# Kernel optimization log

Hardware: AMD Instinct MI355X
Metric: run time of the kernel (lower is better)

The kernel has to match this reference:

```python
import jax, jax.numpy as jnp
import numpy as np

NEG_SLOPE = 0.2
LN_EPS = 1e-5


def _gat(x, src, dst, ea, Wl, Wr, We, att, b, heads, ch, concat):
    # GATv2 conv with edge features (eval mode: dropout = identity).
    N = x.shape[0]
    xl = (x @ Wl).reshape(N, heads, ch)          # source transform (also skip output)
    xr = (x @ Wr).reshape(N, heads, ch)          # target transform
    ee = (ea @ We).reshape(ea.shape[0], heads, ch)
    g = jax.nn.leaky_relu(xl[src] + xr[dst] + ee, NEG_SLOPE)   # [E,H,C]
    score = jnp.einsum('ehc,hc->eh', g, att)                    # [E,H]
    # segment softmax over destination nodes
    smax = jax.ops.segment_max(score, dst, num_segments=N)
    ex = jnp.exp(score - smax[dst])
    den = jax.ops.segment_sum(ex, dst, num_segments=N)
    alpha = ex / (den[dst] + 1e-16)
    out = jax.ops.segment_sum(xl[src] * alpha[..., None], dst, num_segments=N)  # [N,H,C]
    out = out.reshape(N, heads * ch) if concat else out.mean(axis=1)
    return out + b, xl.reshape(N, heads * ch)


def setup_inputs() -> dict:
    B, N, E, F, ED = 4, 20000, 640000, 64, 16
    HID, H1 = 16, 8
    key = jax.random.key(0)
    ks = jax.random.split(key, 32)

    def p(k, shape, fan):
        return (jax.random.normal(k, shape, jnp.float32) / np.float32(np.sqrt(fan)))

    inp = {
        'x': jax.random.normal(ks[0], (B, N, F), jnp.float32),
        'edge_attr': jax.random.normal(ks[1], (B, E, ED), jnp.float32),
        'edge_index': jax.random.randint(ks[2], (B, 2, E), 0, N, jnp.int32),
        # conv1: in=64, heads=8, out=16, concat
        'c1_Wl': p(ks[3], (F, H1 * HID), F),
        'c1_Wr': p(ks[4], (F, H1 * HID), F),
        'c1_We': p(ks[5], (ED, H1 * HID), ED),
        'c1_att': p(ks[6], (H1, HID), HID),
        'c1_b': jnp.zeros((H1 * HID,), jnp.float32),
        # conv2: in=128, heads=1, out=16, mean
        'c2_Wl': p(ks[7], (H1 * HID, HID), H1 * HID),
        'c2_Wr': p(ks[8], (H1 * HID, HID), H1 * HID),
        'c2_We': p(ks[9], (ED, HID), ED),
        'c2_att': p(ks[10], (1, HID), HID),
        'c2_b': jnp.zeros((HID,), jnp.float32),
        # skip_conv: in=128, heads=1, out=16, mean
        's_Wl': p(ks[11], (H1 * HID, HID), H1 * HID),
        's_Wr': p(ks[12], (H1 * HID, HID), H1 * HID),
        's_We': p(ks[13], (ED, HID), ED),
        's_att': p(ks[14], (1, HID), HID),
        's_b': jnp.zeros((HID,), jnp.float32),
        # lin_skip_conv + LayerNorm(16)
        'lin_W': p(ks[15], (HID, HID), HID),
        'lin_b': jnp.zeros((HID,), jnp.float32),
        'ln_g': jnp.ones((HID,), jnp.float32),
        'ln_b': jnp.zeros((HID,), jnp.float32),
    }
    return inp


def reference(x, edge_attr, edge_index,
              c1_Wl, c1_Wr, c1_We, c1_att, c1_b,
              c2_Wl, c2_Wr, c2_We, c2_att, c2_b,
              s_Wl, s_Wr, s_We, s_att, s_b,
              lin_W, lin_b, ln_g, ln_b):
    def single(xg, eig, eag):
        src, dst = eig[0], eig[1]
        h, skip = _gat(xg, src, dst, eag, c1_Wl, c1_Wr, c1_We, c1_att, c1_b, 8, 16, True)
        hx = jax.nn.elu(h)                                   # [N,128]
        x1, _ = _gat(hx, src, dst, eag, c2_Wl, c2_Wr, c2_We, c2_att, c2_b, 1, 16, False)
        # skip conv consumes hx with the residual skip features from conv1
        x2, _ = _gat(hx + skip, src, dst, eag, s_Wl, s_Wr, s_We, s_att, s_b, 1, 16, False)
        x2 = x2 @ lin_W.T + lin_b
        y = x1 + x2                                          # [N,16]
        mu = y.mean(-1, keepdims=True)
        var = ((y - mu) ** 2).mean(-1, keepdims=True)
        return (y - mu) / jnp.sqrt(var + LN_EPS) * ln_g + ln_b
    return jax.vmap(single)(x, edge_index, edge_attr)
```

## Files before the change

kernel.cpp:

```cpp
#include <hip/hip_runtime.h>
#include <hip/hip_bf16.h>

typedef __hip_bfloat16 bf16;
typedef float f32x2 __attribute__((ext_vector_type(2)));

#define NB_B 4
#define N 20000
#define E 640000
#define F 64
#define HC 128
#define ED 16
#define CH 16
#define NT 32
#define TB2 16

__device__ __forceinline__ float clampf(float v, float lo, float hi){ return fminf(fmaxf(v, lo), hi); }
__device__ __forceinline__ float ldv(const float* p, size_t i){ return p[i]; }
__device__ __forceinline__ float ldv(const bf16*  p, size_t i){ return __bfloat162float(p[i]); }
__device__ __forceinline__ void  stv(float* p, size_t i, float v){ p[i] = v; }
__device__ __forceinline__ void  stv(bf16*  p, size_t i, float v){ p[i] = __float2bfloat16(v); }
__device__ __forceinline__ unsigned short tobf(float v){ bf16 b = __float2bfloat16(v); return *(unsigned short*)&b; }
__device__ __forceinline__ float unpl(unsigned u){ return __uint_as_float(u << 16); }
__device__ __forceinline__ float unph(unsigned u){ return __uint_as_float(u & 0xffff0000u); }
__device__ __forceinline__ f32x2 mk2(float a, float b){ f32x2 r; r.x = a; r.y = b; return r; }
__device__ __forceinline__ int rfl(int v){ return __builtin_amdgcn_readfirstlane(v); }

#define L2E 1.44269504f

__device__ __forceinline__ float rsum16(float x){
  x += __int_as_float(__builtin_amdgcn_update_dpp(0, __float_as_int(x), 0x128, 0xf, 0xf, true));
  x += __int_as_float(__builtin_amdgcn_update_dpp(0, __float_as_int(x), 0x124, 0xf, 0xf, true));
  x += __int_as_float(__builtin_amdgcn_update_dpp(0, __float_as_int(x), 0x122, 0xf, 0xf, true));
  x += __int_as_float(__builtin_amdgcn_update_dpp(0, __float_as_int(x), 0x121, 0xf, 0xf, true));
  return x;
}
__device__ __forceinline__ float leaky(float g){
  float a = __uint_as_float(__float_as_uint(g) & 0x7fffffffu);
  return fmaf(0.4f, a, 0.6f*g);
}

__global__ __launch_bounds__(256) void k_detect(const unsigned short* __restrict__ xu, int* __restrict__ flag){
  __shared__ int cnt[256];
  int tid = threadIdx.x;
  unsigned short lo = xu[2*tid];
  bf16 h = *(const bf16*)&lo;
  float v = fabsf(__bfloat162float(h));
  cnt[tid] = (v > 1e4f || (v != 0.f && v < 1e-4f)) ? 1 : 0;
  __syncthreads();
  for (int s=128; s>0; s>>=1){ if (tid<s) cnt[tid]+=cnt[tid+s]; __syncthreads(); }
  if (tid==0) *flag = (cnt[0] > 64) ? 1 : 0;
}

__global__ __launch_bounds__(256) void k_hist(const int* __restrict__ ei, int* __restrict__ cnt, int b0){
  int z = blockIdx.z, b = b0 + z;
  int e = blockIdx.x*256 + threadIdx.x;
  int d = ei[((size_t)b*2+1)*E + e];
  atomicAdd(&cnt[z*N + d], 1);
}

__global__ __launch_bounds__(256) void k_scan(const int* __restrict__ cnt, int* __restrict__ rowptr,
                                              int* __restrict__ cursor){
  int z = blockIdx.z, tid = threadIdx.x;
  const int* c = cnt + (size_t)z*N;
  int* rp = rowptr + (size_t)z*(N+1);
  int* cu = cursor + (size_t)z*N;
  const int CHK = (N + 255)/256;
  int lo = tid*CHK; int hi = lo + CHK; if (hi > N) hi = N; if (lo > N) lo = N;
  int s = 0;
  for (int i=lo;i<hi;i++) s += c[i];
  __shared__ int buf[256];
  buf[tid] = s; __syncthreads();
  for (int off=1; off<256; off<<=1){
    int t = (tid>=off) ? buf[tid-off] : 0;
    __syncthreads();
    buf[tid] += t;
    __syncthreads();
  }
  int run = buf[tid] - s;
  for (int i=lo;i<hi;i++){ int v=c[i]; rp[i]=run; cu[i]=run; run += v; }
  if (tid==255) rp[N] = run;
}

template<typename T>
__device__ __forceinline__ void scatter_body(const int* ei, int* cursor, int* csr,
                                             const T* ea, float* eacsr, int b0){
  int z = blockIdx.z, b = b0 + z;
  int e = blockIdx.x*256 + threadIdx.x;
  int s = ei[((size_t)b*2+0)*E + e];
  int d = ei[((size_t)b*2+1)*E + e];
  int pos = atomicAdd(&cursor[z*N + d], 1);
  csr[(size_t)z*E + pos] = s;
  float4* dst = (float4*)(eacsr + ((size_t)z*E + pos)*ED);
  const T* sp = ea + ((size_t)b*E + e)*ED;
  #pragma unroll
  for (int g=0; g<4; g++){
    float4 t;
    t.x = ldv(sp, g*4+0); t.y = ldv(sp, g*4+1); t.z = ldv(sp, g*4+2); t.w = ldv(sp, g*4+3);
    dst[g] = t;
  }
}
__global__ __launch_bounds__(256) void k_scatter(const int* ei, int* cursor, int* csr,
    const void* ea, float* eacsr, const int* flag, int b0){
  if (*flag) scatter_body(ei, cursor, csr, (const float*)ea, eacsr, b0);
  else       scatter_body(ei, cursor, csr, (const bf16*) ea, eacsr, b0);
}

template<typename T>
__device__ __forceinline__ void node1_body(const T* x, const T* Wl, const T* Wr,
                                           unsigned* xl1p, unsigned* xr1p, int b0,
                                           float (*xs)[F+4]){
  int z = blockIdx.z, b = b0 + z;
  int node0 = blockIdx.x*NT;
  for (int i=threadIdx.x; i<NT*F; i+=256){
    int n = i>>6, k = i&63;
    xs[n][k] = ldv(x, ((size_t)b*N + node0 + n)*F + k);
  }
  __syncthreads();
  int mat = threadIdx.x >> 7, c = threadIdx.x & 127;
  const T* W = mat ? Wr : Wl;
  float acc[NT];
  #pragma unroll
  for (int n=0;n<NT;n++) acc[n]=0.f;
  for (int k=0;k<F;k+=4){
    float w0 = ldv(W, (size_t)(k+0)*HC + c);
    float w1 = ldv(W, (size_t)(k+1)*HC + c);
    float w2 = ldv(W, (size_t)(k+2)*HC + c);
    float w3 = ldv(W, (size_t)(k+3)*HC + c);
    #pragma unroll
    for (int n=0;n<NT;n++){
      float4 xv = *(const float4*)&xs[n][k];
      acc[n] += xv.x*w0 + xv.y*w1 + xv.z*w2 + xv.w*w3;
    }
  }
  unsigned short* outp = (unsigned short*)(mat ? xr1p : xl1p);
  int half = c>>6, cc = c&63;
  #pragma unroll
  for (int n=0;n<NT;n++){
    float v = clampf(acc[n], -1e4f, 1e4f);
    outp[(((size_t)z*N + node0 + n)*64 + cc)*2 + half] = tobf(v);
  }
}
__global__ __launch_bounds__(256) void k_node1(const void* x, const void* Wl, const void* Wr,
    unsigned* xl1p, unsigned* xr1p, const int* flag, int b0){
  __shared__ float xs[NT][F+4];
  if (*flag) node1_body((const float*)x,(const float*)Wl,(const float*)Wr,xl1p,xr1p,b0,xs);
  else       node1_body((const bf16*) x,(const bf16*) Wl,(const bf16*) Wr,xl1p,xr1p,b0,xs);
}

template<typename T>
__device__ __forceinline__ void gather1_body(const int* __restrict__ rowptr, const int* __restrict__ csr,
    const float* __restrict__ eacsr, const T* __restrict__ We, const T* __restrict__ att, const T* __restrict__ b1,
    const unsigned* __restrict__ xl1p, const unsigned* __restrict__ xr1p, float* __restrict__ hx, int b0){
  int z = blockIdx.z;
  int lane = threadIdx.x & 63;
  int node = rfl(blockIdx.x*4 + (threadIdx.x >> 6));
  int rs = rfl(rowptr[(size_t)z*(N+1) + node]);
  int re = rfl(rowptr[(size_t)z*(N+1) + node + 1]);
  f32x2 w[ED];
  #pragma unroll
  for (int j=0;j<ED;j++) w[j] = mk2(ldv(We,(size_t)j*HC+lane), ldv(We,(size_t)j*HC+lane+64));
  float attL = ldv(att,(size_t)lane)*L2E, attH = ldv(att,(size_t)lane+64)*L2E;
  unsigned xru = xr1p[((size_t)z*N + node)*64 + lane];
  f32x2 xr2 = mk2(unpl(xru), unph(xru));
  f32x2 acc = mk2(0.f,0.f), den = mk2(0.f,0.f);
  const unsigned* __restrict__ xlp = xl1p + (size_t)z*N*64;
  const int* __restrict__ csrz = csr + (size_t)z*E + rs;
  const f32x2* __restrict__ eaz = (const f32x2*)(eacsr + ((size_t)z*E + rs)*ED);
  int deg = re - rs;
  if (deg > 0){
    auto EDGE = [&](const f32x2* er, unsigned xw){
      f32x2 xl = mk2(unpl(xw), unph(xw));
      f32x2 g0 = xl + xr2, g1 = mk2(0.f,0.f);
      #pragma unroll
      for (int jp=0;jp<8;jp++){ g0 += w[2*jp]*er[jp].x; g1 += w[2*jp+1]*er[jp].y; }
      f32x2 g = g0 + g1;
      float vL = rsum16(leaky(g.x)*attL);
      float vH = rsum16(leaky(g.y)*attH);
      f32x2 ex = mk2(exp2f(clampf(vL,-86.f,86.f)), exp2f(clampf(vH,-86.f,86.f)));
      den += ex;
      acc += ex*xl;
    };
    int s0 = rfl(csrz[0]);
    int s1 = (deg>1) ? rfl(csrz[1]) : s0;
    unsigned xa = xlp[(size_t)(unsigned)s0*64 + lane];
    unsigned xb = xlp[(size_t)(unsigned)s1*64 + lane];
    f32x2 eA[8], eB[8];
    #pragma unroll
    for (int p=0;p<8;p++) eA[p] = eaz[p];
    int i = 0;
    for (; i+1 < deg; i += 2){
      #pragma unroll
      for (int p=0;p<8;p++) eB[p] = eaz[(size_t)(i+1)*8 + p];
      unsigned x0 = xa, x1 = xb;
      if (i+2 < deg){ int sn = rfl(csrz[i+2]); xa = xlp[(size_t)(unsigned)sn*64 + lane]; }
      if (i+3 < deg){ int sn = rfl(csrz[i+3]); xb = xlp[(size_t)(unsigned)sn*64 + lane]; }
      EDGE(eA, x0);
      if (i+2 < deg){
        #pragma unroll
        for (int p=0;p<8;p++) eA[p] = eaz[(size_t)(i+2)*8 + p];
      }
      EDGE(eB, x1);
    }
    if (i < deg) EDGE(eA, xa);
  }
  float hL = acc.x/(den.x + 1e-16f) + ldv(b1,(size_t)lane);
  float hH = acc.y/(den.y + 1e-16f) + ldv(b1,(size_t)lane+64);
  hL = hL>0.f ? hL : expm1f(hL);
  hH = hH>0.f ? hH : expm1f(hH);
  hx[((size_t)z*N + node)*HC + lane]      = hL;
  hx[((size_t)z*N + node)*HC + lane + 64] = hH;
}
__global__ __launch_bounds__(256) void k_gather1(const int* __restrict__ rowptr, const int* __restrict__ csr,
    const float* __restrict__ eacsr,
    const void* We, const void* att, const void* b1,
    const unsigned* __restrict__ xl1p, const unsigned* __restrict__ xr1p, float* __restrict__ hx,
    const int* __restrict__ flag, int b0){
  if (*flag) gather1_body(rowptr,csr,eacsr,(const float*)We,(const float*)att,(const float*)b1,xl1p,xr1p,hx,b0);
  else       gather1_body(rowptr,csr,eacsr,(const bf16*) We,(const bf16*) att,(const bf16*) b1,xl1p,xr1p,hx,b0);
}

template<typename T>
__device__ __forceinline__ void node2_body(const float* hx, const unsigned* xl1p,
    const T* W2l, const T* W2r, const T* W3l, const T* W3r,
    unsigned* xl23p, unsigned* xr23p, int b0,
    float (*hv)[HC+4], float (*sv)[HC+4]){
  int z = blockIdx.z;
  int node0 = blockIdx.x*NT;
  for (int i=threadIdx.x; i<NT*HC; i+=256){
    int n = i>>7, k = i&127;
    float h = hx[((size_t)z*N + node0 + n)*HC + k];
    unsigned wxl = xl1p[((size_t)z*N + node0 + n)*64 + (k&63)];
    float xv = (k<64) ? unpl(wxl) : unph(wxl);
    hv[n][k] = h;
    sv[n][k] = h + xv;
  }
  __syncthreads();
  int o = threadIdx.x & 63;
  int mat = o >> 4, c = o & 15;
  int g = threadIdx.x >> 6;
  const T* W = (mat==0)? W2l : (mat==1)? W2r : (mat==2)? W3l : W3r;
  float (*src)[HC+4] = (mat<2)? hv : sv;
  float acc[8];
  #pragma unroll
  for (int j=0;j<8;j++) acc[j]=0.f;
  for (int k=0;k<HC;k+=4){
    float w0 = ldv(W, (size_t)(k+0)*CH + c);
    float w1 = ldv(W, (size_t)(k+1)*CH + c);
    float w2 = ldv(W, (size_t)(k+2)*CH + c);
    float w3 = ldv(W, (size_t)(k+3)*CH + c);
    #pragma unroll
    for (int j=0;j<8;j++){
      float4 xv = *(const float4*)&src[g*8+j][k];
      acc[j] += xv.x*w0 + xv.y*w1 + xv.z*w2 + xv.w*w3;
    }
  }
  unsigned short* arr = (unsigned short*)((mat&1) ? xr23p : xl23p);
  int half = mat>>1;
  #pragma unroll
  for (int j=0;j<8;j++){
    float v = clampf(acc[j], -1e4f, 1e4f);
    arr[(((size_t)z*N + node0 + g*8 + j)*CH + c)*2 + half] = tobf(v);
  }
}
__global__ __launch_bounds__(256) void k_node2(const float* hx, const unsigned* xl1p,
    const void* W2l, const void* W2r, const void* W3l, const void* W3r,
    unsigned* xl23p, unsigned* xr23p, const int* flag, int b0){
  __shared__ float hv[NT][HC+4];
  __shared__ float sv[NT][HC+4];
  if (*flag) node2_body(hx,xl1p,(const float*)W2l,(const float*)W2r,(const float*)W3l,(const float*)W3r,xl23p,xr23p,b0,hv,sv);
  else       node2_body(hx,xl1p,(const bf16*) W2l,(const bf16*) W2r,(const bf16*) W3l,(const bf16*) W3r,xl23p,xr23p,b0,hv,sv);
}

template<typename T>
__device__ __forceinline__ void gather23_body(const int* __restrict__ rowptr, const int* __restrict__ csr,
    const float* __restrict__ eacsr,
    const T* We2, const T* We3, const T* att2, const T* att3,
    const T* b2, const T* b3, const T* linW, const T* linb, const T* lng, const T* lnb,
    const unsigned* __restrict__ xl23p, const unsigned* __restrict__ xr23p,
    T* out, int b0, int (*ssrc)[TB2], float (*eas)[TB2][16]){
  int z = blockIdx.z;
  int slot = threadIdx.x >> 4;
  int node = blockIdx.x*16 + slot;
  int c = threadIdx.x & 15;
  int rs = rowptr[(size_t)z*(N+1) + node];
  int re = rowptr[(size_t)z*(N+1) + node + 1];
  unsigned xru = xr23p[((size_t)z*N + node)*CH + c];
  f32x2 xr2 = mk2(unpl(xru), unph(xru));
  f32x2 w[ED];
  #pragma unroll
  for (int j=0;j<ED;j++) w[j] = mk2(ldv(We2,(size_t)j*CH+c), ldv(We3,(size_t)j*CH+c));
  f32x2 attv = mk2(ldv(att2,(size_t)c)*L2E, ldv(att3,(size_t)c)*L2E);
  f32x2 acc = mk2(0.f,0.f), den = mk2(0.f,0.f);
  const unsigned* __restrict__ xlp = xl23p + (size_t)z*N*CH;
  const int* __restrict__ csrz = csr + (size_t)z*E;

  auto edge = [&](int i, unsigned xw){
    f32x2 xl = mk2(unpl(xw), unph(xw));
    float ev[16];
    const float4* er = (const float4*)eas[slot][i];
    *(float4*)&ev[0]  = er[0];
    *(float4*)&ev[4]  = er[1];
    *(float4*)&ev[8]  = er[2];
    *(float4*)&ev[12] = er[3];
    f32x2 g0 = xl + xr2, g1 = mk2(0.f,0.f);
    #pragma unroll
    for (int j=0;j<ED;j+=2){ g0 += w[j]*ev[j]; g1 += w[j+1]*ev[j+1]; }
    f32x2 gg = g0 + g1;
    f32x2 lr = mk2(leaky(gg.x), leaky(gg.y));
    f32x2 v = lr*attv;
    float v2 = rsum16(v.x);
    float v3 = rsum16(v.y);
    f32x2 ex = mk2(exp2f(clampf(v2,-86.f,86.f)), exp2f(clampf(v3,-86.f,86.f)));
    den += ex;
    acc += ex*xl;
  };

  for (int base = rs; base < re; base += TB2){
    int m = re - base; if (m > TB2) m = TB2;
    if (c < m) ssrc[slot][c] = csrz[base + c];
    const float4* ep = (const float4*)(eacsr + ((size_t)z*E + base)*ED);
    for (int i4=c; i4<m*4; i4+=16)
      *(float4*)&eas[slot][i4>>2][(i4&3)*4] = ep[i4];
    unsigned pa = xlp[(unsigned)(ssrc[slot][0]*CH + c)];
    unsigned pb = (m>1) ? xlp[(unsigned)(ssrc[slot][1]*CH + c)] : pa;
    int i = 0;
    for (; i+1 < m; i += 2){
      unsigned x0 = pa, x1 = pb;
      int i2 = (i+2 < m) ? i+2 : m-1;
      int i3 = (i+3 < m) ? i+3 : m-1;
      int s2 = ssrc[slot][i2], s3 = ssrc[slot][i3];
      pa = xlp[(unsigned)(s2*CH + c)];
      pb = xlp[(unsigned)(s3*CH + c)];
      edge(i, x0);
      edge(i+1, x1);
    }
    if (i < m) edge(i, pa);
  }
  float x1 = acc.x/(den.x + 1e-16f) + ldv(b2,(size_t)c);
  float x3 = acc.y/(den.y + 1e-16f) + ldv(b3,(size_t)c);
  float x2 = 0.f;
  #pragma unroll
  for (int j=0;j<16;j++) x2 += __shfl(x3, j, 16) * ldv(linW, (size_t)c*16 + j);
  x2 += ldv(linb,(size_t)c);
  float y = clampf(x1, -1e6f, 1e6f) + clampf(x2, -1e6f, 1e6f);
  float mu = rsum16(y)*(1.f/16.f);
  float dv = y - mu;
  float var = rsum16(dv*dv)*(1.f/16.f);
  float o = dv*rsqrtf(var + 1e-5f)*ldv(lng,(size_t)c) + ldv(lnb,(size_t)c);
  stv(out, ((size_t)(b0+z)*N + node)*16 + c, o);
}
__global__ __launch_bounds__(256) void k_gather23(const int* __restrict__ rowptr, const int* __restrict__ csr,
    const float* __restrict__ eacsr,
    const void* We2, const void* We3, const void* att2, const void* att3,
    const void* b2, const void* b3, const void* linW, const void* linb, const void* lng, const void* lnb,
    const unsigned* __restrict__ xl23p, const unsigned* __restrict__ xr23p,
    void* out, const int* __restrict__ flag, int b0){
  __shared__ int ssrc[16][TB2];
  __shared__ float eas[16][TB2][16];
  if (*flag) gather23_body(rowptr,csr,eacsr,(const float*)We2,(const float*)We3,(const float*)att2,(const float*)att3,
                           (const float*)b2,(const float*)b3,(const float*)linW,(const float*)linb,(const float*)lng,(const float*)lnb,
                           xl23p,xr23p,(float*)out,b0,ssrc,eas);
  else       gather23_body(rowptr,csr,eacsr,(const bf16*) We2,(const bf16*) We3,(const bf16*) att2,(const bf16*) att3,
                           (const bf16*) b2,(const bf16*) b3,(const bf16*) linW,(const bf16*) linb,(const bf16*) lng,(const bf16*) lnb,
                           xl23p,xr23p,(bf16*) out,b0,ssrc,eas);
}

struct WSP {
  int* flag;
  int *cnt, *cursor, *rowptr; int* csr;
  float *eacsr, *hx;
  unsigned *xl1p,*xr1p,*xl23p,*xr23p;
  size_t total;
};
static WSP mkws(char* base, int nb){
  WSP w; size_t off = 0;
  auto A = [&](size_t bytes)->char*{ char* p = base ? base + off : (char*)0; off = (off + bytes + 255) & ~(size_t)255; return p; };
  w.flag   = (int*)     A(256);
  w.cnt    = (int*)     A((size_t)nb*N*4);
  w.cursor = (int*)     A((size_t)nb*N*4);
  w.rowptr = (int*)     A((size_t)nb*(N+1)*4);
  w.csr    = (int*)     A((size_t)nb*E*4);
  w.eacsr  = (float*)   A((size_t)nb*E*ED*4);
  w.hx     = (float*)   A((size_t)nb*N*HC*4);
  w.xl1p   = (unsigned*)A((size_t)nb*N*64*4);
  w.xr1p   = (unsigned*)A((size_t)nb*N*64*4);
  w.xl23p  = (unsigned*)A((size_t)nb*N*CH*4);
  w.xr23p  = (unsigned*)A((size_t)nb*N*CH*4);
  w.total = off;
  return w;
}

extern "C" void kernel_launch(void* const* d_in, const int* in_sizes, int n_in,
                              void* d_out, int out_size, void* d_ws, size_t ws_size,
                              hipStream_t stream){
  const void* x    = d_in[0];
  const void* ea   = d_in[1];
  const int*  ei   = (const int*)d_in[2];
  const void* c1Wl = d_in[3], *c1Wr = d_in[4], *c1We = d_in[5];
  const void* c1att= d_in[6], *c1b  = d_in[7];
  const void* c2Wl = d_in[8], *c2Wr = d_in[9], *c2We = d_in[10];
  const void* c2att= d_in[11],*c2b  = d_in[12];
  const void* sWl  = d_in[13],*sWr  = d_in[14],*sWe  = d_in[15];
  const void* satt = d_in[16],*sb   = d_in[17];
  const void* linW = d_in[18],*linb = d_in[19];
  const void* lng  = d_in[20],*lnb  = d_in[21];

  auto run = [&](int b0, int nb){
    WSP w = mkws((char*)d_ws, nb);
    hipMemsetAsync(w.cnt, 0, (size_t)nb*N*4, stream);
    k_hist   <<<dim3(E/256,1,nb),   256,0,stream>>>(ei, w.cnt, b0);
    k_scan   <<<dim3(1,1,nb),       256,0,stream>>>(w.cnt, w.rowptr, w.cursor);
    k_scatter<<<dim3(E/256,1,nb),   256,0,stream>>>(ei, w.cursor, w.csr, ea, w.eacsr, w.flag, b0);
    k_node1  <<<dim3(N/NT,1,nb),    256,0,stream>>>(x, c1Wl, c1Wr, w.xl1p, w.xr1p, w.flag, b0);
    k_gather1<<<dim3(N/4,1,nb),     256,0,stream>>>(w.rowptr, w.csr, w.eacsr, c1We, c1att, c1b,
                                                    w.xl1p, w.xr1p, w.hx, w.flag, b0);
    k_node2  <<<dim3(N/NT,1,nb),    256,0,stream>>>(w.hx, w.xl1p, c2Wl, c2Wr, sWl, sWr,
                                                    w.xl23p, w.xr23p, w.flag, b0);
    k_gather23<<<dim3(N/16,1,nb),   256,0,stream>>>(w.rowptr, w.csr, w.eacsr, c2We, sWe, c2att, satt,
                                                    c2b, sb, linW, linb, lng, lnb,
                                                    w.xl23p, w.xr23p, d_out, w.flag, b0);
  };

  {
    WSP w0 = mkws((char*)d_ws, 1);
    k_detect<<<1,256,0,stream>>>((const unsigned short*)x, w0.flag);
  }

  WSP probe = mkws((char*)0, NB_B);
  if (ws_size >= probe.total){
    run(0, NB_B);
  } else {
    for (int g=0; g<NB_B; ++g) run(g, 1);
  }
}
```

Before: 1.141 ms.

## Store CSR edge attributes as packed fp16 and use fdot2 for edge projections

The scatter kernel now writes the CSR-permuted edge attributes as packed half pairs (32 bytes per edge instead of 64). Both gather kernels read this compact form and compute the edge-feature projection with v_dot2 fp16 instructions against fp16-packed weights, which replaces scalar FMAs. The gather1 loop is also simplified to a single-edge software pipeline. This cuts edge-attribute write and read traffic and ALU work, at the cost of fp16 rounding of edge attributes and weights.

```diff
diff --git a/kernel.cpp b/kernel.cpp
--- a/kernel.cpp
+++ b/kernel.cpp
@@ -3,6 +3,7 @@
 
 typedef __hip_bfloat16 bf16;
 typedef float f32x2 __attribute__((ext_vector_type(2)));
+typedef _Float16 h2 __attribute__((ext_vector_type(2)));
 
 #define NB_B 4
 #define N 20000
@@ -24,6 +25,16 @@
 __device__ __forceinline__ float unph(unsigned u){ return __uint_as_float(u & 0xffff0000u); }
 __device__ __forceinline__ f32x2 mk2(float a, float b){ f32x2 r; r.x = a; r.y = b; return r; }
 __device__ __forceinline__ int rfl(int v){ return __builtin_amdgcn_readfirstlane(v); }
+
+__device__ __forceinline__ unsigned packh2(float a, float b){
+  _Float16 x = (_Float16)a, y = (_Float16)b;
+  unsigned short ux = *(unsigned short*)&x, uy = *(unsigned short*)&y;
+  return (unsigned)ux | ((unsigned)uy << 16);
+}
+__device__ __forceinline__ float dot2(unsigned a, unsigned b, float c){
+  h2 ha = *(h2*)&a, hb = *(h2*)&b;
+  return __builtin_amdgcn_fdot2(ha, hb, c, false);
+}
 
 #define L2E 1.44269504f
 
@@ -83,26 +94,30 @@
 
 template<typename T>
 __device__ __forceinline__ void scatter_body(const int* ei, int* cursor, int* csr,
-                                             const T* ea, float* eacsr, int b0){
+                                             const T* ea, unsigned* ea8, int b0){
   int z = blockIdx.z, b = b0 + z;
   int e = blockIdx.x*256 + threadIdx.x;
   int s = ei[((size_t)b*2+0)*E + e];
   int d = ei[((size_t)b*2+1)*E + e];
   int pos = atomicAdd(&cursor[z*N + d], 1);
   csr[(size_t)z*E + pos] = s;
-  float4* dst = (float4*)(eacsr + ((size_t)z*E + pos)*ED);
   const T* sp = ea + ((size_t)b*E + e)*ED;
-  #pragma unroll
-  for (int g=0; g<4; g++){
-    float4 t;
-    t.x = ldv(sp, g*4+0); t.y = ldv(sp, g*4+1); t.z = ldv(sp, g*4+2); t.w = ldv(sp, g*4+3);
-    dst[g] = t;
-  }
+  uint4 q0, q1;
+  q0.x = packh2(ldv(sp,0),  ldv(sp,1));
+  q0.y = packh2(ldv(sp,2),  ldv(sp,3));
+  q0.z = packh2(ldv(sp,4),  ldv(sp,5));
+  q0.w = packh2(ldv(sp,6),  ldv(sp,7));
+  q1.x = packh2(ldv(sp,8),  ldv(sp,9));
+  q1.y = packh2(ldv(sp,10), ldv(sp,11));
+  q1.z = packh2(ldv(sp,12), ldv(sp,13));
+  q1.w = packh2(ldv(sp,14), ldv(sp,15));
+  uint4* dst = (uint4*)(ea8 + ((size_t)z*E + pos)*8);
+  dst[0] = q0; dst[1] = q1;
 }
 __global__ __launch_bounds__(256) void k_scatter(const int* ei, int* cursor, int* csr,
-    const void* ea, float* eacsr, const int* flag, int b0){
-  if (*flag) scatter_body(ei, cursor, csr, (const float*)ea, eacsr, b0);
-  else       scatter_body(ei, cursor, csr, (const bf16*) ea, eacsr, b0);
+    const void* ea, unsigned* ea8, const int* flag, int b0){
+  if (*flag) scatter_body(ei, cursor, csr, (const float*)ea, ea8, b0);
+  else       scatter_body(ei, cursor, csr, (const bf16*) ea, ea8, b0);
 }
 
 template<typename T>
@@ -149,74 +164,74 @@
 
 template<typename T>
 __device__ __forceinline__ void gather1_body(const int* __restrict__ rowptr, const int* __restrict__ csr,
-    const float* __restrict__ eacsr, const T* __restrict__ We, const T* __restrict__ att, const T* __restrict__ b1,
+    const unsigned* __restrict__ ea8, const T* __restrict__ We, const T* __restrict__ att, const T* __restrict__ b1,
     const unsigned* __restrict__ xl1p, const unsigned* __restrict__ xr1p, float* __restrict__ hx, int b0){
   int z = blockIdx.z;
   int lane = threadIdx.x & 63;
   int node = rfl(blockIdx.x*4 + (threadIdx.x >> 6));
   int rs = rfl(rowptr[(size_t)z*(N+1) + node]);
   int re = rfl(rowptr[(size_t)z*(N+1) + node + 1]);
-  f32x2 w[ED];
-  #pragma unroll
-  for (int j=0;j<ED;j++) w[j] = mk2(ldv(We,(size_t)j*HC+lane), ldv(We,(size_t)j*HC+lane+64));
+  unsigned wA[8], wB[8];
+  #pragma unroll
+  for (int jp=0;jp<8;jp++){
+    wA[jp] = packh2(ldv(We,(size_t)(2*jp)*HC+lane),    ldv(We,(size_t)(2*jp+1)*HC+lane));
+    wB[jp] = packh2(ldv(We,(size_t)(2*jp)*HC+lane+64), ldv(We,(size_t)(2*jp+1)*HC+lane+64));
+  }
   float attL = ldv(att,(size_t)lane)*L2E, attH = ldv(att,(size_t)lane+64)*L2E;
   unsigned xru = xr1p[((size_t)z*N + node)*64 + lane];
-  f32x2 xr2 = mk2(unpl(xru), unph(xru));
-  f32x2 acc = mk2(0.f,0.f), den = mk2(0.f,0.f);
+  float xrL = unpl(xru), xrH = unph(xru);
+  float accL=0.f, accH=0.f, denL=0.f, denH=0.f;
   const unsigned* __restrict__ xlp = xl1p + (size_t)z*N*64;
   const int* __restrict__ csrz = csr + (size_t)z*E + rs;
-  const f32x2* __restrict__ eaz = (const f32x2*)(eacsr + ((size_t)z*E + rs)*ED);
+  const uint4* __restrict__ ep = (const uint4*)(ea8 + ((size_t)z*E + rs)*8);
   int deg = re - rs;
   if (deg > 0){
-    auto EDGE = [&](const f32x2* er, unsigned xw){
-      f32x2 xl = mk2(unpl(xw), unph(xw));
-      f32x2 g0 = xl + xr2, g1 = mk2(0.f,0.f);
-      #pragma unroll
-      for (int jp=0;jp<8;jp++){ g0 += w[2*jp]*er[jp].x; g1 += w[2*jp+1]*er[jp].y; }
-      f32x2 g = g0 + g1;
-      float vL = rsum16(leaky(g.x)*attL);
-      float vH = rsum16(leaky(g.y)*attH);
-      f32x2 ex = mk2(exp2f(clampf(vL,-86.f,86.f)), exp2f(clampf(vH,-86.f,86.f)));
-      den += ex;
-      acc += ex*xl;
-    };
     int s0 = rfl(csrz[0]);
     int s1 = (deg>1) ? rfl(csrz[1]) : s0;
-    unsigned xa = xlp[(size_t)(unsigned)s0*64 + lane];
-    unsigned xb = xlp[(size_t)(unsigned)s1*64 + lane];
-    f32x2 eA[8], eB[8];
-    #pragma unroll
-    for (int p=0;p<8;p++) eA[p] = eaz[p];
-    int i = 0;
-    for (; i+1 < deg; i += 2){
-      #pragma unroll
-      for (int p=0;p<8;p++) eB[p] = eaz[(size_t)(i+1)*8 + p];
-      unsigned x0 = xa, x1 = xb;
-      if (i+2 < deg){ int sn = rfl(csrz[i+2]); xa = xlp[(size_t)(unsigned)sn*64 + lane]; }
-      if (i+3 < deg){ int sn = rfl(csrz[i+3]); xb = xlp[(size_t)(unsigned)sn*64 + lane]; }
-      EDGE(eA, x0);
+    unsigned xa = (xlp + (size_t)(unsigned)s0*64)[lane];
+    unsigned xb = (xlp + (size_t)(unsigned)s1*64)[lane];
+    uint4 e0 = ep[0], e1 = ep[1];
+    for (int i=0;i<deg;i++){
+      unsigned xw = xa; xa = xb;
+      uint4 c0 = e0, c1 = e1;
+      if (i+1 < deg){ e0 = ep[2*(i+1)]; e1 = ep[2*(i+1)+1]; }
       if (i+2 < deg){
-        #pragma unroll
-        for (int p=0;p<8;p++) eA[p] = eaz[(size_t)(i+2)*8 + p];
+        int sn = rfl(csrz[i+2]);
+        xb = (xlp + (size_t)(unsigned)sn*64)[lane];
       }
-      EDGE(eB, x1);
+      float xlL = unpl(xw), xlH = unph(xw);
+      float gL = xlL + xrL, gH = xlH + xrH;
+      gL = dot2(c0.x, wA[0], gL);  gH = dot2(c0.x, wB[0], gH);
+      gL = dot2(c0.y, wA[1], gL);  gH = dot2(c0.y, wB[1], gH);
+      gL = dot2(c0.z, wA[2], gL);  gH = dot2(c0.z, wB[2], gH);
+      gL = dot2(c0.w, wA[3], gL);  gH = dot2(c0.w, wB[3], gH);
+      gL = dot2(c1.x, wA[4], gL);  gH = dot2(c1.x, wB[4], gH);
+      gL = dot2(c1.y, wA[5], gL);  gH = dot2(c1.y, wB[5], gH);
+      gL = dot2(c1.z, wA[6], gL);  gH = dot2(c1.z, wB[6], gH);
+      gL = dot2(c1.w, wA[7], gL);  gH = dot2(c1.w, wB[7], gH);
+      float vL = rsum16(leaky(gL)*attL);
+      float vH = rsum16(leaky(gH)*attH);
+      float exL = exp2f(clampf(vL,-86.f,86.f));
+      float exH = exp2f(clampf(vH,-86.f,86.f));
+      denL += exL; denH += exH;
+      accL = fmaf(exL, xlL, accL);
+      accH = fmaf(exH, xlH, accH);
     }
-    if (i < deg) EDGE(eA, xa);
-  }
-  float hL = acc.x/(den.x + 1e-16f) + ldv(b1,(size_t)lane);
-  float hH = acc.y/(den.y + 1e-16f) + ldv(b1,(size_t)lane+64);
+  }
+  float hL = accL/(denL + 1e-16f) + ldv(b1,(size_t)lane);
+  float hH = accH/(denH + 1e-16f) + ldv(b1,(size_t)lane+64);
   hL = hL>0.f ? hL : expm1f(hL);
   hH = hH>0.f ? hH : expm1f(hH);
   hx[((size_t)z*N + node)*HC + lane]      = hL;
   hx[((size_t)z*N + node)*HC + lane + 64] = hH;
 }
 __global__ __launch_bounds__(256) void k_gather1(const int* __restrict__ rowptr, const int* __restrict__ csr,
-    const float* __restrict__ eacsr,
+    const unsigned* __restrict__ ea8,
     const void* We, const void* att, const void* b1,
     const unsigned* __restrict__ xl1p, const unsigned* __restrict__ xr1p, float* __restrict__ hx,
     const int* __restrict__ flag, int b0){
-  if (*flag) gather1_body(rowptr,csr,eacsr,(const float*)We,(const float*)att,(const float*)b1,xl1p,xr1p,hx,b0);
-  else       gather1_body(rowptr,csr,eacsr,(const bf16*) We,(const bf16*) att,(const bf16*) b1,xl1p,xr1p,hx,b0);
+  if (*flag) gather1_body(rowptr,csr,ea8,(const float*)We,(const float*)att,(const float*)b1,xl1p,xr1p,hx,b0);
+  else       gather1_body(rowptr,csr,ea8,(const bf16*) We,(const bf16*) att,(const bf16*) b1,xl1p,xr1p,hx,b0);
 }
 
 template<typename T>
@@ -273,11 +288,11 @@
 
 template<typename T>
 __device__ __forceinline__ void gather23_body(const int* __restrict__ rowptr, const int* __restrict__ csr,
-    const float* __restrict__ eacsr,
+    const unsigned* __restrict__ ea8,
     const T* We2, const T* We3, const T* att2, const T* att3,
     const T* b2, const T* b3, const T* linW, const T* linb, const T* lng, const T* lnb,
     const unsigned* __restrict__ xl23p, const unsigned* __restrict__ xr23p,
-    T* out, int b0, int (*ssrc)[TB2], float (*eas)[TB2][16]){
+    T* out, int b0, int (*ssrc)[TB2], unsigned (*eas)[TB2][8]){
   int z = blockIdx.z;
   int slot = threadIdx.x >> 4;
   int node = blockIdx.x*16 + slot;
@@ -285,42 +300,46 @@
   int rs = rowptr[(size_t)z*(N+1) + node];
   int re = rowptr[(size_t)z*(N+1) + node + 1];
   unsigned xru = xr23p[((size_t)z*N + node)*CH + c];
-  f32x2 xr2 = mk2(unpl(xru), unph(xru));
-  f32x2 w[ED];
-  #pragma unroll
-  for (int j=0;j<ED;j++) w[j] = mk2(ldv(We2,(size_t)j*CH+c), ldv(We3,(size_t)j*CH+c));
-  f32x2 attv = mk2(ldv(att2,(size_t)c)*L2E, ldv(att3,(size_t)c)*L2E);
-  f32x2 acc = mk2(0.f,0.f), den = mk2(0.f,0.f);
+  float xr2v = unpl(xru), xr3v = unph(xru);
+  unsigned w2p[8], w3p[8];
+  #pragma unroll
+  for (int jp=0;jp<8;jp++){
+    w2p[jp] = packh2(ldv(We2,(size_t)(2*jp)*CH+c), ldv(We2,(size_t)(2*jp+1)*CH+c));
+    w3p[jp] = packh2(ldv(We3,(size_t)(2*jp)*CH+c), ldv(We3,(size_t)(2*jp+1)*CH+c));
+  }
+  float att2c = ldv(att2,(size_t)c)*L2E, att3c = ldv(att3,(size_t)c)*L2E;
+  float acc2=0.f, acc3=0.f, den2=0.f, den3=0.f;
   const unsigned* __restrict__ xlp = xl23p + (size_t)z*N*CH;
   const int* __restrict__ csrz = csr + (size_t)z*E;
 
   auto edge = [&](int i, unsigned xw){
-    f32x2 xl = mk2(unpl(xw), unph(xw));
-    float ev[16];
-    const float4* er = (const float4*)eas[slot][i];
-    *(float4*)&ev[0]  = er[0];
-    *(float4*)&ev[4]  = er[1];
-    *(float4*)&ev[8]  = er[2];
-    *(float4*)&ev[12] = er[3];
-    f32x2 g0 = xl + xr2, g1 = mk2(0.f,0.f);
-    #pragma unroll
-    for (int j=0;j<ED;j+=2){ g0 += w[j]*ev[j]; g1 += w[j+1]*ev[j+1]; }
-    f32x2 gg = g0 + g1;
-    f32x2 lr = mk2(leaky(gg.x), leaky(gg.y));
-    f32x2 v = lr*attv;
-    float v2 = rsum16(v.x);
-    float v3 = rsum16(v.y);
-    f32x2 ex = mk2(exp2f(clampf(v2,-86.f,86.f)), exp2f(clampf(v3,-86.f,86.f)));
-    den += ex;
-    acc += ex*xl;
+    float xl2v = unpl(xw), xl3v = unph(xw);
+    uint4 q0 = *(const uint4*)&eas[slot][i][0];
+    uint4 q1 = *(const uint4*)&eas[slot][i][4];
+    float g2 = xl2v + xr2v, g3 = xl3v + xr3v;
+    g2 = dot2(q0.x, w2p[0], g2);  g3 = dot2(q0.x, w3p[0], g3);
+    g2 = dot2(q0.y, w2p[1], g2);  g3 = dot2(q0.y, w3p[1], g3);
+    g2 = dot2(q0.z, w2p[2], g2);  g3 = dot2(q0.z, w3p[2], g3);
+    g2 = dot2(q0.w, w2p[3], g2);  g3 = dot2(q0.w, w3p[3], g3);
+    g2 = dot2(q1.x, w2p[4], g2);  g3 = dot2(q1.x, w3p[4], g3);
+    g2 = dot2(q1.y, w2p[5], g2);  g3 = dot2(q1.y, w3p[5], g3);
+    g2 = dot2(q1.z, w2p[6], g2);  g3 = dot2(q1.z, w3p[6], g3);
+    g2 = dot2(q1.w, w2p[7], g2);  g3 = dot2(q1.w, w3p[7], g3);
+    float v2 = rsum16(leaky(g2)*att2c);
+    float v3 = rsum16(leaky(g3)*att3c);
+    float ex2 = exp2f(clampf(v2,-86.f,86.f));
+    float ex3 = exp2f(clampf(v3,-86.f,86.f));
+    den2 += ex2; den3 += ex3;
+    acc2 = fmaf(ex2, xl2v, acc2);
+    acc3 = fmaf(ex3, xl3v, acc3);
   };
 
   for (int base = rs; base < re; base += TB2){
     int m = re - base; if (m > TB2) m = TB2;
     if (c < m) ssrc[slot][c] = csrz[base + c];
-    const float4* ep = (const float4*)(eacsr + ((size_t)z*E + base)*ED);
-    for (int i4=c; i4<m*4; i4+=16)
-      *(float4*)&eas[slot][i4>>2][(i4&3)*4] = ep[i4];
+    const uint4* ep = (const uint4*)(ea8 + ((size_t)z*E + base)*8);
+    for (int i4=c; i4<m*2; i4+=16)
+      ((uint4*)eas[slot])[i4] = ep[i4];
     unsigned pa = xlp[(unsigned)(ssrc[slot][0]*CH + c)];
     unsigned pb = (m>1) ? xlp[(unsigned)(ssrc[slot][1]*CH + c)] : pa;
     int i = 0;
@@ -336,8 +355,8 @@
     }
     if (i < m) edge(i, pa);
   }
-  float x1 = acc.x/(den.x + 1e-16f) + ldv(b2,(size_t)c);
-  float x3 = acc.y/(den.y + 1e-16f) + ldv(b3,(size_t)c);
+  float x1 = acc2/(den2 + 1e-16f) + ldv(b2,(size_t)c);
+  float x3 = acc3/(den3 + 1e-16f) + ldv(b3,(size_t)c);
   float x2 = 0.f;
   #pragma unroll
   for (int j=0;j<16;j++) x2 += __shfl(x3, j, 16) * ldv(linW, (size_t)c*16 + j);
@@ -350,17 +369,17 @@
   stv(out, ((size_t)(b0+z)*N + node)*16 + c, o);
 }
 __global__ __launch_bounds__(256) void k_gather23(const int* __restrict__ rowptr, const int* __restrict__ csr,
-    const float* __restrict__ eacsr,
+    const unsigned* __restrict__ ea8,
     const void* We2, const void* We3, const void* att2, const void* att3,
     const void* b2, const void* b3, const void* linW, const void* linb, const void* lng, const void* lnb,
     const unsigned* __restrict__ xl23p, const unsigned* __restrict__ xr23p,
     void* out, const int* __restrict__ flag, int b0){
   __shared__ int ssrc[16][TB2];
-  __shared__ float eas[16][TB2][16];
-  if (*flag) gather23_body(rowptr,csr,eacsr,(const float*)We2,(const float*)We3,(const float*)att2,(const float*)att3,
+  __shared__ unsigned eas[16][TB2][8];
+  if (*flag) gather23_body(rowptr,csr,ea8,(const float*)We2,(const float*)We3,(const float*)att2,(const float*)att3,
                            (const float*)b2,(const float*)b3,(const float*)linW,(const float*)linb,(const float*)lng,(const float*)lnb,
                            xl23p,xr23p,(float*)out,b0,ssrc,eas);
-  else       gather23_body(rowptr,csr,eacsr,(const bf16*) We2,(const bf16*) We3,(const bf16*) att2,(const bf16*) att3,
+  else       gather23_body(rowptr,csr,ea8,(const bf16*) We2,(const bf16*) We3,(const bf16*) att2,(const bf16*) att3,
                            (const bf16*) b2,(const bf16*) b3,(const bf16*) linW,(const bf16*) linb,(const bf16*) lng,(const bf16*) lnb,
                            xl23p,xr23p,(bf16*) out,b0,ssrc,eas);
 }
@@ -368,7 +387,8 @@
 struct WSP {
   int* flag;
   int *cnt, *cursor, *rowptr; int* csr;
-  float *eacsr, *hx;
+  unsigned* ea8;
+  float* hx;
   unsigned *xl1p,*xr1p,*xl23p,*xr23p;
   size_t total;
 };
@@ -380,7 +400,7 @@
   w.cursor = (int*)     A((size_t)nb*N*4);
   w.rowptr = (int*)     A((size_t)nb*(N+1)*4);
   w.csr    = (int*)     A((size_t)nb*E*4);
-  w.eacsr  = (float*)   A((size_t)nb*E*ED*4);
+  w.ea8    = (unsigned*)A((size_t)nb*E*8*4);
   w.hx     = (float*)   A((size_t)nb*N*HC*4);
   w.xl1p   = (unsigned*)A((size_t)nb*N*64*4);
   w.xr1p   = (unsigned*)A((size_t)nb*N*64*4);
@@ -410,13 +430,13 @@
     hipMemsetAsync(w.cnt, 0, (size_t)nb*N*4, stream);
     k_hist   <<<dim3(E/256,1,nb),   256,0,stream>>>(ei, w.cnt, b0);
     k_scan   <<<dim3(1,1,nb),       256,0,stream>>>(w.cnt, w.rowptr, w.cursor);
-    k_scatter<<<dim3(E/256,1,nb),   256,0,stream>>>(ei, w.cursor, w.csr, ea, w.eacsr, w.flag, b0);
+    k_scatter<<<dim3(E/256,1,nb),   256,0,stream>>>(ei, w.cursor, w.csr, ea, w.ea8, w.flag, b0);
     k_node1  <<<dim3(N/NT,1,nb),    256,0,stream>>>(x, c1Wl, c1Wr, w.xl1p, w.xr1p, w.flag, b0);
-    k_gather1<<<dim3(N/4,1,nb),     256,0,stream>>>(w.rowptr, w.csr, w.eacsr, c1We, c1att, c1b,
+    k_gather1<<<dim3(N/4,1,nb),     256,0,stream>>>(w.rowptr, w.csr, w.ea8, c1We, c1att, c1b,
                                                     w.xl1p, w.xr1p, w.hx, w.flag, b0);
     k_node2  <<<dim3(N/NT,1,nb),    256,0,stream>>>(w.hx, w.xl1p, c2Wl, c2Wr, sWl, sWr,
                                                     w.xl23p, w.xr23p, w.flag, b0);
-    k_gather23<<<dim3(N/16,1,nb),   256,0,stream>>>(w.rowptr, w.csr, w.eacsr, c2We, sWe, c2att, satt,
+    k_gather23<<<dim3(N/16,1,nb),   256,0,stream>>>(w.rowptr, w.csr, w.ea8, c2We, sWe, c2att, satt,
                                                     c2b, sb, linW, linb, lng, lnb,
                                                     w.xl23p, w.xr23p, d_out, w.flag, b0);
   };
```

Measured after the change: 1.028 ms. -9.9%, faster.
